# Kernel tuning notes

Hardware: AMD Instinct MI355X
Metric: run time of the kernel (lower is better)

The kernel has to match this reference:

```python
import jax, jax.numpy as jnp
import numpy as np

B, T, C, A, D, H, W = 2, 16, 64, 64, 32, 32, 32  # batch, timepoints, channels, att_features, spatial


def setup_inputs() -> dict:
    key = jax.random.key(0)
    ks = jax.random.split(key, 7)
    s = 1.0 / np.sqrt(C)
    return {
        "x": jax.random.normal(ks[0], (B, T, C, D, H, W), dtype=jnp.float32),
        "Wk": jax.random.normal(ks[1], (A, C), dtype=jnp.float32) * s,
        "bk": jax.random.normal(ks[2], (A,), dtype=jnp.float32) * s,
        "Wq": jax.random.normal(ks[3], (A, C), dtype=jnp.float32) * s,
        "bq": jax.random.normal(ks[4], (A,), dtype=jnp.float32) * s,
        "Wv": jax.random.normal(ks[5], (C, C), dtype=jnp.float32) * s,
        "bv": jax.random.normal(ks[6], (C,), dtype=jnp.float32) * s,
    }


def reference(x, Wk, bk, Wq, bq, Wv, bv):
    # kernel=1 Conv3d == pointwise channel mixing. Project and move spatial
    # dims to the front exactly like movedim((3,4,5),(1,2,3)):
    # result layout [B, D, H, W, T, out_ch].
    def proj(Wt, bt):
        return jnp.einsum('btcdhw,oc->bdhwto', x, Wt) + bt

    k = proj(Wk, bk)  # [B,D,H,W,T,A]
    q = proj(Wq, bq)  # [B,D,H,W,T,A]
    v = proj(Wv, bv)  # [B,D,H,W,T,C]

    scale = 1.0 / np.sqrt(float(Wk.shape[0]))  # sqrt(att_features)
    att = jnp.einsum('bdhwta,bdhwsa->bdhwts', k, q) * scale  # [B,D,H,W,T,T]
    # norm = partial(softmax, dim=1) on the 6-D tensor -> softmax over spatial D axis
    att_map = jax.nn.softmax(att, axis=1)

    # features = (value^T @ att_map)^T: feat[...,s,c] = sum_t v[...,t,c] * att_map[...,t,s]
    feat = jnp.einsum('bdhwtc,bdhwts->bdhwsc', v, att_map)  # [B,D,H,W,T,C]
    # movedim((1,2,3),(3,4,5)): back to [B, T, C, D, H, W]
    return jnp.transpose(feat, (0, 4, 5, 1, 2, 3))
```

## Files before the change

### kernel.cpp

```cpp
#include <hip/hip_runtime.h>

typedef short v8s __attribute__((ext_vector_type(8)));
typedef float v4f __attribute__((ext_vector_type(4)));
typedef float v2f __attribute__((ext_vector_type(2)));

#define NSP 32768
#define XSTR 2056
#define WS_ZP_B 65536ull

__device__ __forceinline__ unsigned short f2bf(float f) {
  union { float f; unsigned u; } v; v.f = f;
  unsigned r = v.u + 0x7fffu + ((v.u >> 16) & 1u);
  return (unsigned short)(r >> 16);
}
__device__ __forceinline__ unsigned pk(float a, float b) {
  return (unsigned)f2bf(a) | ((unsigned)f2bf(b) << 16);
}

union UF8 { v8s v; unsigned u[4]; uint4 q; };


__global__ __launch_bounds__(512) void prep_kernel(
    const float* __restrict__ Wk, const float* __restrict__ bk,
    const float* __restrict__ Wq, const float* __restrict__ bq,
    const float* __restrict__ Wv, unsigned* __restrict__ ws) {
  __shared__ float sWk[4096], sWq[4096], sWv[4096], sbk[64], sbq[64];
  for (int i = threadIdx.x; i < 4096; i += 512) { sWk[i] = Wk[i]; sWq[i] = Wq[i]; sWv[i] = Wv[i]; }
  if (threadIdx.x < 64) { sbk[threadIdx.x] = bk[threadIdx.x]; sbq[threadIdx.x] = bq[threadIdx.x]; }
  __syncthreads();
  for (int task = threadIdx.x; task < 18 * 64; task += 512) {
    int f = task >> 6, lane = task & 63;
    int i16 = lane & 15, g = lane >> 4;
    unsigned short e[8];
    #pragma unroll
    for (int j = 0; j < 8; ++j) {
      int k = (((j >> 2) << 4) + 4 * g + (j & 3));
      float acc = 0.f;
      if (f < 8) {
        int row = ((f >> 1) << 4) + i16;
        int cc  = ((f & 1) << 5) + k;
        for (int a = 0; a < 64; ++a) acc += sWk[a * 64 + row] * sWq[a * 64 + cc];
      } else if (f < 10) {
        int c = ((f - 8) << 5) + k;
        if (i16 == 0)      { for (int a = 0; a < 64; ++a) acc += sWk[a * 64 + c] * sbq[a]; }
        else if (i16 == 1) { for (int a = 0; a < 64; ++a) acc += sbk[a] * sWq[a * 64 + c]; }
      } else {
        int c  = (((f - 10) >> 1) << 4) + i16;
        int cp = (((f - 10) & 1) << 5) + k;
        acc = sWv[c * 64 + cp];
      }
      e[j] = f2bf(acc);
    }
    unsigned* dst = ws + (size_t)(f * 64 + lane) * 4;
    dst[0] = e[0] | ((unsigned)e[1] << 16);
    dst[1] = e[2] | ((unsigned)e[3] << 16);
    dst[2] = e[4] | ((unsigned)e[5] << 16);
    dst[3] = e[6] | ((unsigned)e[7] << 16);
  }
  if (threadIdx.x == 0) {
    float beta = 0.f;
    for (int a = 0; a < 64; ++a) beta += sbk[a] * sbq[a];
    ((float*)ws)[18 * 256] = beta;
  }
}

#define S2L 0.18033688011112042f

#define DECODE256() \
  int bid = (int)blockIdx.x; \
  int b = bid & 1, dc = (bid >> 1) & 3, h = bid >> 3; \
  const int d0 = dc << 3; \
  const size_t base0 = (size_t)b * 33554432 + h * 32;

#define DECODE512() \
  int bid = (int)blockIdx.x; \
  int b = bid & 1, dcc = (bid >> 1) & 7, h = bid >> 4; \
  const int d0 = dcc << 2; \
  const size_t base0 = (size_t)b * 33554432 + h * 32;

#define STAGE_DEFS() \
  const int w2 = tid & 15; \
  const int rp0 = tid >> 4; \
  v2f sA[8], sB[8]; \
  auto issueH = [&](int d, int half) { \
    const float* xp = x + base0 + (size_t)d * 1024; \
    _Pragma("unroll") \
    for (int i = 0; i < 8; ++i) { \
      int rp = half * 256 + (i << 5) + rp0; \
      const float* r0 = xp + (size_t)(2 * rp) * NSP + 2 * w2; \
      sA[i] = *(const v2f*)r0; \
      sB[i] = *(const v2f*)(r0 + NSP); \
    } \
  }; \
  auto writeH = [&](unsigned char* BUF, int half) { \
    _Pragma("unroll") \
    for (int i = 0; i < 8; ++i) { \
      int rp = half * 256 + (i << 5) + rp0; \
      int t = rp >> 5, c = (rp & 31) << 1; \
      int off = (t << 7) + (((c << 1)) ^ ((t & 7) << 4)); \
      *(unsigned*)(&BUF[(2 * w2) * XSTR + off])     = pk(sA[i].x, sB[i].x); \
      *(unsigned*)(&BUF[(2 * w2 + 1) * XSTR + off]) = pk(sA[i].y, sB[i].y); \
    } \
  };

#define LOADX_DEF() \
  auto loadX = [&](const unsigned char* BUF, int loc, v8s fX[2]) { \
    const unsigned char* bp = &BUF[loc * XSTR + (i16 << 7)]; \
    const int sw = (i16 & 7) << 4; \
    _Pragma("unroll") \
    for (int kc = 0; kc < 2; ++kc) { \
      union { v8s v; unsigned long long dd[2]; } u; \
      int o = (kc << 6) + (g << 3); \
      u.dd[0] = *(const unsigned long long*)(bp + (o ^ sw)); \
      u.dd[1] = *(const unsigned long long*)(bp + ((o + 32) ^ sw)); \
      fX[kc] = u.v; \
    } \
  };

#define LDF_DEF() \
  auto ldf = [&](int f) -> v8s { \
    union { v8s v; uint4 q; } u; \
    u.q = *(const uint4*)&Wm[(f << 8) + (lane << 2)]; \
    return u.v; \
  };

#define ATTOF_DEF() \
  auto attOf = [&](const v8s fX[2]) -> v4f { \
    v4f accW[4]; \
    _Pragma("unroll") \
    for (int tr = 0; tr < 4; ++tr) { \
      v8s m0 = ldf(2 * tr), m1 = ldf(2 * tr + 1); \
      v4f a = {0.f, 0.f, 0.f, 0.f}; \
      a = __builtin_amdgcn_mfma_f32_16x16x32_bf16(m0, fX[0], a, 0, 0, 0); \
      a = __builtin_amdgcn_mfma_f32_16x16x32_bf16(m1, fX[1], a, 0, 0, 0); \
      accW[tr] = a; \
    } \
    v8s u0 = ldf(8), u1 = ldf(9); \
    v4f au = {0.f, 0.f, 0.f, 0.f}; \
    au = __builtin_amdgcn_mfma_f32_16x16x32_bf16(u0, fX[0], au, 0, 0, 0); \
    au = __builtin_amdgcn_mfma_f32_16x16x32_bf16(u1, fX[1], au, 0, 0, 0); \
    float a1v = au[0] + beta; \
    float a2v = au[1]; \
    float a2s = __shfl(a2v, i16); \
    v4f att; \
    _Pragma("unroll") \
    for (int j = 0; j < 4; ++j) att[j] = __shfl(a1v, 4 * g + j) + a2s; \
    _Pragma("unroll") \
    for (int kc = 0; kc < 2; ++kc) { \
      UF8 w; \
      w.u[0] = pk(accW[2 * kc][0], accW[2 * kc][1]); \
      w.u[1] = pk(accW[2 * kc][2], accW[2 * kc][3]); \
      w.u[2] = pk(accW[2 * kc + 1][0], accW[2 * kc + 1][1]); \
      w.u[3] = pk(accW[2 * kc + 1][2], accW[2 * kc + 1][3]); \
      att = __builtin_amdgcn_mfma_f32_16x16x32_bf16(fX[kc], w.v, att, 0, 0, 0); \
    } \
    return att; \
  };

#define FEATQ(tn, FB) do { \
  _Pragma("unroll") \
  for (int l = 0; l < 4; ++l) { \
    int wq = 4 * wv + l; \
    UF8 fP; fP.u[0] = Pp[l][0]; fP.u[1] = Pp[l][1]; fP.u[2] = 0; fP.u[3] = 0; \
    UF8 fV; fV.u[0] = vp[l][2 * (tn)]; fV.u[1] = vp[l][2 * (tn) + 1]; fV.u[2] = 0; fV.u[3] = 0; \
    v4f ft = {0.f, 0.f, 0.f, 0.f}; \
    ft = __builtin_amdgcn_mfma_f32_16x16x32_bf16(fP.v, fV.v, ft, 0, 0, 0); \
    _Pragma("unroll") \
    for (int j = 0; j < 4; ++j) { \
      int r = (4 * g + j) * 16 + i16; \
      (FB)[r * 33 + (wq ^ g)] = ft[j]; \
    } \
  } \
} while (0)

__global__ __launch_bounds__(512) void pass1_z(
    const float* __restrict__ x, const unsigned* __restrict__ ws,
    float* __restrict__ zp) {
  __shared__ __align__(16) unsigned char Xd[2][65792];
  __shared__ unsigned Wm[2560];

  const int tid = (int)threadIdx.x;
  const int lane = tid & 63, wv = tid >> 6;
  const int i16 = lane & 15, g = lane >> 4;
  DECODE256();

  for (int o = tid; o < 2560; o += 512) Wm[o] = ws[o];
  const float beta = ((const float*)ws)[4608];

  STAGE_DEFS();
  LOADX_DEF();
  LDF_DEF();
  ATTOF_DEF();

  float Z[4][4] = {};
  issueH(d0, 0); writeH(Xd[0], 0);
  issueH(d0, 1); writeH(Xd[0], 1);
  __syncthreads();
  for (int ii = 0; ii < 8; ++ii) {
    const int d = d0 + ii;
    unsigned char* cur = Xd[ii & 1];
    unsigned char* nxt = Xd[(ii & 1) ^ 1];
    if (ii < 7) issueH(d + 1, 0);
    #pragma unroll
    for (int l = 0; l < 2; ++l) {
      v8s fX[2]; loadX(cur, 4 * wv + l, fX);
      v4f att = attOf(fX);
      #pragma unroll
      for (int j = 0; j < 4; ++j) Z[l][j] += exp2f(att[j] * S2L);
    }
    if (ii < 7) { writeH(nxt, 0); issueH(d + 1, 1); }
    #pragma unroll
    for (int l = 2; l < 4; ++l) {
      v8s fX[2]; loadX(cur, 4 * wv + l, fX);
      v4f att = attOf(fX);
      #pragma unroll
      for (int j = 0; j < 4; ++j) Z[l][j] += exp2f(att[j] * S2L);
    }
    if (ii < 7) writeH(nxt, 1);
    __syncthreads();
  }
  const int locg = b * 1024 + h * 32 + 4 * wv;
  #pragma unroll
  for (int l = 0; l < 4; ++l)
    #pragma unroll
    for (int j = 0; j < 4; ++j)
      zp[(((size_t)dc * 2048 + locg + l) << 8) + (4 * g + j) * 16 + i16] = Z[l][j];
}

__global__ __launch_bounds__(512) void pass2_out(
    const float* __restrict__ x, const float* __restrict__ bv,
    const unsigned* __restrict__ ws, const float* __restrict__ zp,
    float* __restrict__ out) {
  __shared__ __align__(16) unsigned char Xd[2][67584];
  __shared__ unsigned Wm[4608];

  const int tid = (int)threadIdx.x;
  const int lane = tid & 63, wv = tid >> 6;
  const int i16 = lane & 15, g = lane >> 4;
  DECODE512();

  for (int o = tid; o < 4608; o += 512) Wm[o] = ws[o];
  const float beta = ((const float*)ws)[4608];
  float bvv[4];
  #pragma unroll
  for (int tn = 0; tn < 4; ++tn) bvv[tn] = bv[i16 + 16 * tn];

  float iZ[4][4];
  #pragma unroll
  for (int l = 0; l < 4; ++l) {
    const int locg = b * 1024 + h * 32 + 4 * wv + l;
    #pragma unroll
    for (int j = 0; j < 4; ++j) {
      float s = 0.f;
      #pragma unroll
      for (int c2 = 0; c2 < 4; ++c2)
        s += zp[(((size_t)c2 * 2048 + locg) << 8) + (4 * g + j) * 16 + i16];
      iZ[l][j] = 1.f / s;
    }
  }

  STAGE_DEFS();
  LOADX_DEF();
  LDF_DEF();
  ATTOF_DEF();

  auto storeQ = [&](int tn, int d, const float* FB) {
    float* op = out + base0 + (size_t)d * 1024 + (size_t)(16 * tn) * NSP;
    const int w4 = tid & 7, rr = tid >> 3;
    #pragma unroll
    for (int it = 0; it < 4; ++it) {
      int r = (it << 6) + rr;
      const float* fp = &FB[r * 33 + (w4 << 2)];
      float4 val;
      val.x = fp[0 ^ it]; val.y = fp[1 ^ it]; val.z = fp[2 ^ it]; val.w = fp[3 ^ it];
      *(float4*)(op + (size_t)((r >> 4) * 64 + (r & 15)) * NSP + (w4 << 2)) = val;
    }
  };

  issueH(d0, 0); writeH(Xd[0], 0);
  issueH(d0, 1); writeH(Xd[0], 1);
  for (int ii = 0; ii < 4; ++ii) {
    const int d = d0 + ii;
    unsigned char* A = Xd[ii & 1];
    unsigned char* B = Xd[(ii & 1) ^ 1];
    __syncthreads();

    unsigned Pp[4][2], vp[4][8];
    if (ii < 3) issueH(d + 1, 0);
    #pragma unroll
    for (int l = 0; l < 4; ++l) {
      if (l == 2 && ii < 3) { writeH(B, 0); issueH(d + 1, 1); }
      v8s fX[2]; loadX(A, 4 * wv + l, fX);
      v4f att = attOf(fX);
      float p0 = exp2f(att[0] * S2L) * iZ[l][0];
      float p1 = exp2f(att[1] * S2L) * iZ[l][1];
      float p2 = exp2f(att[2] * S2L) * iZ[l][2];
      float p3 = exp2f(att[3] * S2L) * iZ[l][3];
      Pp[l][0] = pk(p0, p1); Pp[l][1] = pk(p2, p3);
      #pragma unroll
      for (int tn = 0; tn < 4; ++tn) {
        v8s wa = ldf(10 + 2 * tn), wb = ldf(11 + 2 * tn);
        v4f a = {bvv[tn], bvv[tn], bvv[tn], bvv[tn]};
        a = __builtin_amdgcn_mfma_f32_16x16x32_bf16(fX[0], wa, a, 0, 0, 0);
        a = __builtin_amdgcn_mfma_f32_16x16x32_bf16(fX[1], wb, a, 0, 0, 0);
        vp[l][2 * tn] = pk(a[0], a[1]); vp[l][2 * tn + 1] = pk(a[2], a[3]);
      }
    }
    if (ii < 3) writeH(B, 1);
    __syncthreads();

    float* FbA = (float*)A;
    float* FbB = FbA + 8448;
    FEATQ(0, FbA);
    __syncthreads();
    storeQ(0, d, FbA); FEATQ(1, FbB);
    __syncthreads();
    storeQ(1, d, FbB); FEATQ(2, FbA);
    __syncthreads();
    storeQ(2, d, FbA); FEATQ(3, FbB);
    __syncthreads();
    storeQ(3, d, FbB);
  }
}

extern "C" void kernel_launch(void* const* d_in, const int* in_sizes, int n_in,
                              void* d_out, int out_size, void* d_ws, size_t ws_size,
                              hipStream_t stream) {
  const float* x  = (const float*)d_in[0];
  const float* Wk = (const float*)d_in[1];
  const float* bk = (const float*)d_in[2];
  const float* bq = (const float*)d_in[4];
  const float* Wq = (const float*)d_in[3];
  const float* Wv = (const float*)d_in[5];
  const float* bv = (const float*)d_in[6];
  float* out = (float*)d_out;
  unsigned* ws = (unsigned*)d_ws;
  float* zp = (float*)((char*)d_ws + WS_ZP_B);

  prep_kernel<<<1, 512, 0, stream>>>(Wk, bk, Wq, bq, Wv, ws);
  pass1_z<<<256, 512, 0, stream>>>(x, ws, zp);
  pass2_out<<<512, 512, 0, stream>>>(x, bv, ws, zp, out);
}
```

Measured before the change: 267.7 us.

## Halve per-block W tile to raise occupancy and grid size in both passes

Both passes now split each H row into two 16-wide W halves, so each block covers half as many spatial locations. This halves the shared staging buffers (about 66KB instead of 132KB), which allows more resident blocks per CU, and both grids grow to 1024 blocks. Pass 1 now uses 4-deep D chunks, giving 8 partial Z sums that pass 2 reduces. Pass 2 reads the value-projection weights straight from global memory instead of LDS and uses a new XOR-swizzled feature buffer layout with float4 reads. The cost is more staging overhead relative to the work per block, narrower 32-byte global row segments, and more partial-sum reads.

Result: slower. 359.9 us (+34.5%).

```diff
diff --git a/kernel.cpp b/kernel.cpp
--- a/kernel.cpp
+++ b/kernel.cpp
@@ -66,27 +66,24 @@
 
 #define S2L 0.18033688011112042f
 
-#define DECODE256() \
+#define DECODE1024() \
   int bid = (int)blockIdx.x; \
-  int b = bid & 1, dc = (bid >> 1) & 3, h = bid >> 3; \
-  const int d0 = dc << 3; \
-  const size_t base0 = (size_t)b * 33554432 + h * 32;
-
-#define DECODE512() \
-  int bid = (int)blockIdx.x; \
-  int b = bid & 1, dcc = (bid >> 1) & 7, h = bid >> 4; \
+  int b   = bid & 1; \
+  int whp = (bid >> 3) & 1; \
+  int dcc = ((bid >> 1) & 3) | (((bid >> 4) & 1) << 2); \
+  int h   = bid >> 5; \
   const int d0 = dcc << 2; \
-  const size_t base0 = (size_t)b * 33554432 + h * 32;
+  const size_t base0 = (size_t)b * 33554432 + h * 32 + whp * 16;
 
 #define STAGE_DEFS() \
-  const int w2 = tid & 15; \
-  const int rp0 = tid >> 4; \
-  v2f sA[8], sB[8]; \
+  const int w2 = tid & 7; \
+  const int rp0 = tid >> 3; \
+  v2f sA[4], sB[4]; \
   auto issueH = [&](int d, int half) { \
     const float* xp = x + base0 + (size_t)d * 1024; \
     _Pragma("unroll") \
-    for (int i = 0; i < 8; ++i) { \
-      int rp = half * 256 + (i << 5) + rp0; \
+    for (int i = 0; i < 4; ++i) { \
+      int rp = half * 256 + (i << 6) + rp0; \
       const float* r0 = xp + (size_t)(2 * rp) * NSP + 2 * w2; \
       sA[i] = *(const v2f*)r0; \
       sB[i] = *(const v2f*)(r0 + NSP); \
@@ -94,8 +91,8 @@
   }; \
   auto writeH = [&](unsigned char* BUF, int half) { \
     _Pragma("unroll") \
-    for (int i = 0; i < 8; ++i) { \
-      int rp = half * 256 + (i << 5) + rp0; \
+    for (int i = 0; i < 4; ++i) { \
+      int rp = half * 256 + (i << 6) + rp0; \
       int t = rp >> 5, c = (rp & 31) << 1; \
       int off = (t << 7) + (((c << 1)) ^ ((t & 7) << 4)); \
       *(unsigned*)(&BUF[(2 * w2) * XSTR + off])     = pk(sA[i].x, sB[i].x); \
@@ -159,8 +156,8 @@
 
 #define FEATQ(tn, FB) do { \
   _Pragma("unroll") \
-  for (int l = 0; l < 4; ++l) { \
-    int wq = 4 * wv + l; \
+  for (int l = 0; l < 2; ++l) { \
+    int wq = 2 * wv + l; \
     UF8 fP; fP.u[0] = Pp[l][0]; fP.u[1] = Pp[l][1]; fP.u[2] = 0; fP.u[3] = 0; \
     UF8 fV; fV.u[0] = vp[l][2 * (tn)]; fV.u[1] = vp[l][2 * (tn) + 1]; fV.u[2] = 0; fV.u[3] = 0; \
     v4f ft = {0.f, 0.f, 0.f, 0.f}; \
@@ -168,7 +165,7 @@
     _Pragma("unroll") \
     for (int j = 0; j < 4; ++j) { \
       int r = (4 * g + j) * 16 + i16; \
-      (FB)[r * 33 + (wq ^ g)] = ft[j]; \
+      (FB)[r * 16 + (wq ^ (((g + (i16 >> 1)) & 3) << 2))] = ft[j]; \
     } \
   } \
 } while (0)
@@ -176,13 +173,13 @@
 __global__ __launch_bounds__(512) void pass1_z(
     const float* __restrict__ x, const unsigned* __restrict__ ws,
     float* __restrict__ zp) {
-  __shared__ __align__(16) unsigned char Xd[2][65792];
+  __shared__ __align__(16) unsigned char Xd[2][32896];
   __shared__ unsigned Wm[2560];
 
   const int tid = (int)threadIdx.x;
   const int lane = tid & 63, wv = tid >> 6;
   const int i16 = lane & 15, g = lane >> 4;
-  DECODE256();
+  DECODE1024();
 
   for (int o = tid; o < 2560; o += 512) Wm[o] = ws[o];
   const float beta = ((const float*)ws)[4608];
@@ -192,68 +189,67 @@
   LDF_DEF();
   ATTOF_DEF();
 
-  float Z[4][4] = {};
+  float Z[2][4] = {};
   issueH(d0, 0); writeH(Xd[0], 0);
   issueH(d0, 1); writeH(Xd[0], 1);
   __syncthreads();
-  for (int ii = 0; ii < 8; ++ii) {
+  for (int ii = 0; ii < 4; ++ii) {
     const int d = d0 + ii;
     unsigned char* cur = Xd[ii & 1];
     unsigned char* nxt = Xd[(ii & 1) ^ 1];
-    if (ii < 7) issueH(d + 1, 0);
-    #pragma unroll
-    for (int l = 0; l < 2; ++l) {
-      v8s fX[2]; loadX(cur, 4 * wv + l, fX);
+    if (ii < 3) issueH(d + 1, 0);
+    {
+      v8s fX[2]; loadX(cur, 2 * wv, fX);
       v4f att = attOf(fX);
       #pragma unroll
-      for (int j = 0; j < 4; ++j) Z[l][j] += exp2f(att[j] * S2L);
-    }
-    if (ii < 7) { writeH(nxt, 0); issueH(d + 1, 1); }
-    #pragma unroll
-    for (int l = 2; l < 4; ++l) {
-      v8s fX[2]; loadX(cur, 4 * wv + l, fX);
+      for (int j = 0; j < 4; ++j) Z[0][j] += exp2f(att[j] * S2L);
+    }
+    if (ii < 3) { writeH(nxt, 0); issueH(d + 1, 1); }
+    {
+      v8s fX[2]; loadX(cur, 2 * wv + 1, fX);
       v4f att = attOf(fX);
       #pragma unroll
-      for (int j = 0; j < 4; ++j) Z[l][j] += exp2f(att[j] * S2L);
-    }
-    if (ii < 7) writeH(nxt, 1);
-    __syncthreads();
-  }
-  const int locg = b * 1024 + h * 32 + 4 * wv;
+      for (int j = 0; j < 4; ++j) Z[1][j] += exp2f(att[j] * S2L);
+    }
+    if (ii < 3) writeH(nxt, 1);
+    __syncthreads();
+  }
   #pragma unroll
-  for (int l = 0; l < 4; ++l)
+  for (int l = 0; l < 2; ++l) {
+    const int locg = b * 1024 + h * 32 + whp * 16 + 2 * wv + l;
     #pragma unroll
     for (int j = 0; j < 4; ++j)
-      zp[(((size_t)dc * 2048 + locg + l) << 8) + (4 * g + j) * 16 + i16] = Z[l][j];
+      zp[(((size_t)dcc * 2048 + locg) << 8) + (4 * g + j) * 16 + i16] = Z[l][j];
+  }
 }
 
 __global__ __launch_bounds__(512) void pass2_out(
     const float* __restrict__ x, const float* __restrict__ bv,
     const unsigned* __restrict__ ws, const float* __restrict__ zp,
     float* __restrict__ out) {
-  __shared__ __align__(16) unsigned char Xd[2][67584];
-  __shared__ unsigned Wm[4608];
+  __shared__ __align__(16) unsigned char Xd[2][32896];
+  __shared__ unsigned Wm[2560];
 
   const int tid = (int)threadIdx.x;
   const int lane = tid & 63, wv = tid >> 6;
   const int i16 = lane & 15, g = lane >> 4;
-  DECODE512();
-
-  for (int o = tid; o < 4608; o += 512) Wm[o] = ws[o];
+  DECODE1024();
+
+  for (int o = tid; o < 2560; o += 512) Wm[o] = ws[o];
   const float beta = ((const float*)ws)[4608];
   float bvv[4];
   #pragma unroll
   for (int tn = 0; tn < 4; ++tn) bvv[tn] = bv[i16 + 16 * tn];
 
-  float iZ[4][4];
+  float iZ[2][4];
   #pragma unroll
-  for (int l = 0; l < 4; ++l) {
-    const int locg = b * 1024 + h * 32 + 4 * wv + l;
+  for (int l = 0; l < 2; ++l) {
+    const int locg = b * 1024 + h * 32 + whp * 16 + 2 * wv + l;
     #pragma unroll
     for (int j = 0; j < 4; ++j) {
       float s = 0.f;
       #pragma unroll
-      for (int c2 = 0; c2 < 4; ++c2)
+      for (int c2 = 0; c2 < 8; ++c2)
         s += zp[(((size_t)c2 * 2048 + locg) << 8) + (4 * g + j) * 16 + i16];
       iZ[l][j] = 1.f / s;
     }
@@ -264,16 +260,17 @@
   LDF_DEF();
   ATTOF_DEF();
 
+  const uint4* W4 = (const uint4*)ws;
+
   auto storeQ = [&](int tn, int d, const float* FB) {
     float* op = out + base0 + (size_t)d * 1024 + (size_t)(16 * tn) * NSP;
-    const int w4 = tid & 7, rr = tid >> 3;
-    #pragma unroll
-    for (int it = 0; it < 4; ++it) {
-      int r = (it << 6) + rr;
-      const float* fp = &FB[r * 33 + (w4 << 2)];
-      float4 val;
-      val.x = fp[0 ^ it]; val.y = fp[1 ^ it]; val.z = fp[2 ^ it]; val.w = fp[3 ^ it];
-      *(float4*)(op + (size_t)((r >> 4) * 64 + (r & 15)) * NSP + (w4 << 2)) = val;
+    const int w4 = tid & 3, rr = tid >> 2;
+    #pragma unroll
+    for (int it = 0; it < 2; ++it) {
+      int r = (it << 7) + rr;
+      int q = ((r >> 6) + ((r & 15) >> 1)) & 3;
+      float4 val = *(const float4*)&FB[r * 16 + 4 * w4];
+      *(float4*)(op + (size_t)(((r >> 4) << 6) + (r & 15)) * NSP + 4 * (w4 ^ q)) = val;
     }
   };
 
@@ -285,12 +282,12 @@
     unsigned char* B = Xd[(ii & 1) ^ 1];
     __syncthreads();
 
-    unsigned Pp[4][2], vp[4][8];
+    unsigned Pp[2][2], vp[2][8];
     if (ii < 3) issueH(d + 1, 0);
     #pragma unroll
-    for (int l = 0; l < 4; ++l) {
-      if (l == 2 && ii < 3) { writeH(B, 0); issueH(d + 1, 1); }
-      v8s fX[2]; loadX(A, 4 * wv + l, fX);
+    for (int l = 0; l < 2; ++l) {
+      if (l == 1 && ii < 3) { writeH(B, 0); issueH(d + 1, 1); }
+      v8s fX[2]; loadX(A, 2 * wv + l, fX);
       v4f att = attOf(fX);
       float p0 = exp2f(att[0] * S2L) * iZ[l][0];
       float p1 = exp2f(att[1] * S2L) * iZ[l][1];
@@ -299,10 +296,12 @@
       Pp[l][0] = pk(p0, p1); Pp[l][1] = pk(p2, p3);
       #pragma unroll
       for (int tn = 0; tn < 4; ++tn) {
-        v8s wa = ldf(10 + 2 * tn), wb = ldf(11 + 2 * tn);
+        UF8 wa, wb;
+        wa.q = W4[(10 + 2 * tn) * 64 + lane];
+        wb.q = W4[(11 + 2 * tn) * 64 + lane];
         v4f a = {bvv[tn], bvv[tn], bvv[tn], bvv[tn]};
-        a = __builtin_amdgcn_mfma_f32_16x16x32_bf16(fX[0], wa, a, 0, 0, 0);
-        a = __builtin_amdgcn_mfma_f32_16x16x32_bf16(fX[1], wb, a, 0, 0, 0);
+        a = __builtin_amdgcn_mfma_f32_16x16x32_bf16(fX[0], wa.v, a, 0, 0, 0);
+        a = __builtin_amdgcn_mfma_f32_16x16x32_bf16(fX[1], wb.v, a, 0, 0, 0);
         vp[l][2 * tn] = pk(a[0], a[1]); vp[l][2 * tn + 1] = pk(a[2], a[3]);
       }
     }
@@ -310,7 +309,7 @@
     __syncthreads();
 
     float* FbA = (float*)A;
-    float* FbB = FbA + 8448;
+    float* FbB = FbA + 4096;
     FEATQ(0, FbA);
     __syncthreads();
     storeQ(0, d, FbA); FEATQ(1, FbB);
@@ -329,8 +328,8 @@
   const float* x  = (const float*)d_in[0];
   const float* Wk = (const float*)d_in[1];
   const float* bk = (const float*)d_in[2];
+  const float* Wq = (const float*)d_in[3];
   const float* bq = (const float*)d_in[4];
-  const float* Wq = (const float*)d_in[3];
   const float* Wv = (const float*)d_in[5];
   const float* bv = (const float*)d_in[6];
   float* out = (float*)d_out;
@@ -338,6 +337,6 @@
   float* zp = (float*)((char*)d_ws + WS_ZP_B);
 
   prep_kernel<<<1, 512, 0, stream>>>(Wk, bk, Wq, bq, Wv, ws);
-  pass1_z<<<256, 512, 0, stream>>>(x, ws, zp);
-  pass2_out<<<512, 512, 0, stream>>>(x, bv, ws, zp, out);
-}
+  pass1_z<<<1024, 512, 0, stream>>>(x, ws, zp);
+  pass2_out<<<1024, 512, 0, stream>>>(x, bv, ws, zp, out);
+}
```

## Cache scaled attention logits in fp16 from pass1 for reuse in pass2

Applied to the files above, without the earlier changes.

Pass1 now writes the scaled attention logits for every location to a workspace buffer in fp16 while it accumulates the softmax denominators. Pass2 reads these logits back instead of recomputing the K/Q attention MFMAs, and only loads the value weights into shared memory. The next depth's logits are prefetched during the store phase. This trades recomputing attention for roughly 16 MB of extra global write and read traffic, and the fp16 rounding of logits could slightly change accuracy.

Result: slower. 274.1 us (+2.4%).

```diff
diff --git a/kernel.cpp b/kernel.cpp
--- a/kernel.cpp
+++ b/kernel.cpp
@@ -1,4 +1,5 @@
 #include <hip/hip_runtime.h>
+#include <hip/hip_fp16.h>
 
 typedef short v8s __attribute__((ext_vector_type(8)));
 typedef float v4f __attribute__((ext_vector_type(4)));
@@ -6,7 +7,8 @@
 
 #define NSP 32768
 #define XSTR 2056
-#define WS_ZP_B 65536ull
+#define WS_ZP_B  65536ull
+#define WS_ATT_B 16777216ull
 
 __device__ __forceinline__ unsigned short f2bf(float f) {
   union { float f; unsigned u; } v; v.f = f;
@@ -15,6 +17,12 @@
 }
 __device__ __forceinline__ unsigned pk(float a, float b) {
   return (unsigned)f2bf(a) | ((unsigned)f2bf(b) << 16);
+}
+__device__ __forceinline__ unsigned pkh(float a, float b) {
+  union { __half2 h; unsigned u; } c; c.h = __floats2half2_rn(a, b); return c.u;
+}
+__device__ __forceinline__ float2 uph(unsigned u) {
+  union { unsigned u; __half2 h; } c; c.u = u; return __half22float2(c.h);
 }
 
 union UF8 { v8s v; unsigned u[4]; uint4 q; };
@@ -175,7 +183,7 @@
 
 __global__ __launch_bounds__(512) void pass1_z(
     const float* __restrict__ x, const unsigned* __restrict__ ws,
-    float* __restrict__ zp) {
+    float* __restrict__ zp, unsigned* __restrict__ attw) {
   __shared__ __align__(16) unsigned char Xd[2][65792];
   __shared__ unsigned Wm[2560];
 
@@ -191,6 +199,18 @@
   LOADX_DEF();
   LDF_DEF();
   ATTOF_DEF();
+
+  auto doLoc = [&](const unsigned char* cur, int d, int l, float Zl[4]) {
+    v8s fX[2]; loadX(cur, 4 * wv + l, fX);
+    v4f att = attOf(fX);
+    float s0 = att[0] * S2L, s1 = att[1] * S2L;
+    float s2 = att[2] * S2L, s3 = att[3] * S2L;
+    Zl[0] += exp2f(s0); Zl[1] += exp2f(s1);
+    Zl[2] += exp2f(s2); Zl[3] += exp2f(s3);
+    uint2 av; av.x = pkh(s0, s1); av.y = pkh(s2, s3);
+    const size_t ls = ((size_t)((b << 5) + h) * 32 + d) * 32 + (4 * wv + l);
+    *(uint2*)(attw + ls * 128 + lane * 2) = av;
+  };
 
   float Z[4][4] = {};
   issueH(d0, 0); writeH(Xd[0], 0);
@@ -201,21 +221,11 @@
     unsigned char* cur = Xd[ii & 1];
     unsigned char* nxt = Xd[(ii & 1) ^ 1];
     if (ii < 7) issueH(d + 1, 0);
-    #pragma unroll
-    for (int l = 0; l < 2; ++l) {
-      v8s fX[2]; loadX(cur, 4 * wv + l, fX);
-      v4f att = attOf(fX);
-      #pragma unroll
-      for (int j = 0; j < 4; ++j) Z[l][j] += exp2f(att[j] * S2L);
-    }
+    doLoc(cur, d, 0, Z[0]);
+    doLoc(cur, d, 1, Z[1]);
     if (ii < 7) { writeH(nxt, 0); issueH(d + 1, 1); }
-    #pragma unroll
-    for (int l = 2; l < 4; ++l) {
-      v8s fX[2]; loadX(cur, 4 * wv + l, fX);
-      v4f att = attOf(fX);
-      #pragma unroll
-      for (int j = 0; j < 4; ++j) Z[l][j] += exp2f(att[j] * S2L);
-    }
+    doLoc(cur, d, 2, Z[2]);
+    doLoc(cur, d, 3, Z[3]);
     if (ii < 7) writeH(nxt, 1);
     __syncthreads();
   }
@@ -230,17 +240,16 @@
 __global__ __launch_bounds__(512) void pass2_out(
     const float* __restrict__ x, const float* __restrict__ bv,
     const unsigned* __restrict__ ws, const float* __restrict__ zp,
-    float* __restrict__ out) {
+    const unsigned* __restrict__ attw, float* __restrict__ out) {
   __shared__ __align__(16) unsigned char Xd[2][67584];
-  __shared__ unsigned Wm[4608];
+  __shared__ unsigned Wm[2048];
 
   const int tid = (int)threadIdx.x;
   const int lane = tid & 63, wv = tid >> 6;
   const int i16 = lane & 15, g = lane >> 4;
   DECODE512();
 
-  for (int o = tid; o < 4608; o += 512) Wm[o] = ws[o];
-  const float beta = ((const float*)ws)[4608];
+  for (int o = tid; o < 2048; o += 512) Wm[o] = ws[2560 + o];
   float bvv[4];
   #pragma unroll
   for (int tn = 0; tn < 4; ++tn) bvv[tn] = bv[i16 + 16 * tn];
@@ -261,8 +270,19 @@
 
   STAGE_DEFS();
   LOADX_DEF();
-  LDF_DEF();
-  ATTOF_DEF();
+
+  auto lfv = [&](int f) -> v8s {
+    union { v8s v; uint4 q; } u;
+    u.q = *(const uint4*)&Wm[(f << 8) + (lane << 2)];
+    return u.v;
+  };
+  auto loadAtt = [&](int d, uint2* dst) {
+    #pragma unroll
+    for (int l = 0; l < 4; ++l) {
+      const size_t ls = ((size_t)((b << 5) + h) * 32 + d) * 32 + (4 * wv + l);
+      dst[l] = *(const uint2*)(attw + ls * 128 + lane * 2);
+    }
+  };
 
   auto storeQ = [&](int tn, int d, const float* FB) {
     float* op = out + base0 + (size_t)d * 1024 + (size_t)(16 * tn) * NSP;
@@ -277,6 +297,8 @@
     }
   };
 
+  uint2 ar[4];
+  loadAtt(d0, ar);
   issueH(d0, 0); writeH(Xd[0], 0);
   issueH(d0, 1); writeH(Xd[0], 1);
   for (int ii = 0; ii < 4; ++ii) {
@@ -290,16 +312,14 @@
     #pragma unroll
     for (int l = 0; l < 4; ++l) {
       if (l == 2 && ii < 3) { writeH(B, 0); issueH(d + 1, 1); }
+      float2 f01 = uph(ar[l].x), f23 = uph(ar[l].y);
+      float p0 = exp2f(f01.x) * iZ[l][0], p1 = exp2f(f01.y) * iZ[l][1];
+      float p2 = exp2f(f23.x) * iZ[l][2], p3 = exp2f(f23.y) * iZ[l][3];
+      Pp[l][0] = pk(p0, p1); Pp[l][1] = pk(p2, p3);
       v8s fX[2]; loadX(A, 4 * wv + l, fX);
-      v4f att = attOf(fX);
-      float p0 = exp2f(att[0] * S2L) * iZ[l][0];
-      float p1 = exp2f(att[1] * S2L) * iZ[l][1];
-      float p2 = exp2f(att[2] * S2L) * iZ[l][2];
-      float p3 = exp2f(att[3] * S2L) * iZ[l][3];
-      Pp[l][0] = pk(p0, p1); Pp[l][1] = pk(p2, p3);
       #pragma unroll
       for (int tn = 0; tn < 4; ++tn) {
-        v8s wa = ldf(10 + 2 * tn), wb = ldf(11 + 2 * tn);
+        v8s wa = lfv(2 * tn), wb = lfv(2 * tn + 1);
         v4f a = {bvv[tn], bvv[tn], bvv[tn], bvv[tn]};
         a = __builtin_amdgcn_mfma_f32_16x16x32_bf16(fX[0], wa, a, 0, 0, 0);
         a = __builtin_amdgcn_mfma_f32_16x16x32_bf16(fX[1], wb, a, 0, 0, 0);
@@ -311,15 +331,19 @@
 
     float* FbA = (float*)A;
     float* FbB = FbA + 8448;
+    uint2 arN[4];
     FEATQ(0, FbA);
     __syncthreads();
-    storeQ(0, d, FbA); FEATQ(1, FbB);
+    storeQ(0, d, FbA);
+    if (ii < 3) loadAtt(d + 1, arN);
+    FEATQ(1, FbB);
     __syncthreads();
     storeQ(1, d, FbB); FEATQ(2, FbA);
     __syncthreads();
     storeQ(2, d, FbA); FEATQ(3, FbB);
     __syncthreads();
     storeQ(3, d, FbB);
+    if (ii < 3) { ar[0] = arN[0]; ar[1] = arN[1]; ar[2] = arN[2]; ar[3] = arN[3]; }
   }
 }
 
@@ -329,15 +353,16 @@
   const float* x  = (const float*)d_in[0];
   const float* Wk = (const float*)d_in[1];
   const float* bk = (const float*)d_in[2];
+  const float* Wq = (const float*)d_in[3];
   const float* bq = (const float*)d_in[4];
-  const float* Wq = (const float*)d_in[3];
   const float* Wv = (const float*)d_in[5];
   const float* bv = (const float*)d_in[6];
   float* out = (float*)d_out;
   unsigned* ws = (unsigned*)d_ws;
-  float* zp = (float*)((char*)d_ws + WS_ZP_B);
+  float*    zp   = (float*)((char*)d_ws + WS_ZP_B);
+  unsigned* attw = (unsigned*)((char*)d_ws + WS_ATT_B);
 
   prep_kernel<<<1, 512, 0, stream>>>(Wk, bk, Wq, bq, Wv, ws);
-  pass1_z<<<256, 512, 0, stream>>>(x, ws, zp);
-  pass2_out<<<512, 512, 0, stream>>>(x, bv, ws, zp, out);
-}
+  pass1_z<<<256, 512, 0, stream>>>(x, ws, zp, attw);
+  pass2_out<<<512, 512, 0, stream>>>(x, bv, ws, zp, attw, out);
+}
```
